# Performance work log

Measured on AMD Instinct MI355X. Metric: run time of the kernel, lower is better.

The kernel has to match this reference:

```python
import jax, jax.numpy as jnp
import numpy as np

B, T, C = 2, 2048, 2048
NH = 16            # query heads
NKV = NH // 2      # kv heads (GQA)
HD = C // NH       # head dim = 128
N_REP = NH // NKV  # 2


def setup_inputs() -> dict:
    key = jax.random.key(0)
    k1, k2, k3 = jax.random.split(key, 3)
    x = jax.random.normal(k1, (B, T, C), jnp.float32)
    w_attn = jax.random.normal(k2, (C, (NH + 2 * NKV) * HD), jnp.float32) * 0.02
    w_proj = jax.random.normal(k3, (C, C), jnp.float32) * 0.02
    t = jnp.arange(T, dtype=jnp.float32)
    inv_freq = 1.0 / (10000.0 ** (jnp.arange(0, HD, 2, dtype=jnp.float32) / HD))
    freqs = t[:, None] * inv_freq[None, :]  # [T, HD//2]
    return {"x": x, "w_attn": w_attn, "w_proj": w_proj,
            "freqs_cos": jnp.cos(freqs), "freqs_sin": jnp.sin(freqs)}


def _rope(v, cos, sin):
    # v: [B, T, H, HD]; complex multiply on (even, odd) pairs
    vr = v.reshape(*v.shape[:-1], HD // 2, 2)
    x0, x1 = vr[..., 0], vr[..., 1]
    c = cos[None, :, None, :]
    s = sin[None, :, None, :]
    o0 = x0 * c - x1 * s
    o1 = x0 * s + x1 * c
    return jnp.stack([o0, o1], axis=-1).reshape(v.shape)


def reference(x, w_attn, w_proj, freqs_cos, freqs_sin):
    qkv = x @ w_attn  # [B, T, (NH+2*NKV)*HD]
    q, k, v = jnp.split(qkv, [NH * HD, (NH + NKV) * HD], axis=-1)
    q = q.reshape(B, T, NH, HD)
    k = k.reshape(B, T, NKV, HD)
    v = v.reshape(B, T, NKV, HD)
    q = _rope(q, freqs_cos, freqs_sin)
    k = _rope(k, freqs_cos, freqs_sin)
    # GQA: group query heads over kv heads instead of repeating k/v
    q = q.transpose(0, 2, 1, 3).reshape(B, NKV, N_REP, T, HD)  # [B, G, R, T, HD]
    k = k.transpose(0, 2, 1, 3)  # [B, G, T, HD]
    v = v.transpose(0, 2, 1, 3)  # [B, G, T, HD]
    scale = jnp.float32(1.0 / np.sqrt(HD))
    scores = jnp.einsum('bgrqd,bgkd->bgrqk', q, k) * scale
    causal = jnp.tril(jnp.ones((T, T), dtype=bool))
    scores = jnp.where(causal, scores, jnp.float32(-1e30))
    p = jax.nn.softmax(scores, axis=-1)
    y = jnp.einsum('bgrqk,bgkd->bgrqd', p, v)  # [B, G, R, T, HD]
    y = y.reshape(B, NH, T, HD).transpose(0, 2, 1, 3).reshape(B, T, C)
    return y @ w_proj
```

## Files before the change

### kernel.cpp

```cpp
#include <hip/hip_runtime.h>
#include <hip/hip_bf16.h>
#include <stdint.h>
#include <stddef.h>

typedef unsigned short u16;
using bf16x8 = __attribute__((ext_vector_type(8))) short;
using f32x4  = __attribute__((ext_vector_type(4))) float;

#define DEVFN static __device__ __forceinline__

DEVFN u16 f2b(float f){ __hip_bfloat16 h = __float2bfloat16(f); return *reinterpret_cast<u16*>(&h); }
DEVFN float b2f(u16 u){ __hip_bfloat16 h; *reinterpret_cast<u16*>(&h) = u; return __bfloat162float(h); }

DEVFN void gload_lds16(const void* g, void* l){
  __builtin_amdgcn_global_load_lds(
      (const __attribute__((address_space(1))) void*)g,
      (__attribute__((address_space(3))) void*)l, 16, 0, 0);
}

__global__ void detect_k(const uint32_t* __restrict__ fc_raw, uint32_t* __restrict__ flag){
  if (threadIdx.x == 0 && blockIdx.x == 0)
    flag[0] = (fc_raw[0] == 0x3F800000u) ? 1u : 0u;
}

__global__ __launch_bounds__(256) void cvtf_k(const void* __restrict__ in, float* __restrict__ out,
                                              int n, const uint32_t* __restrict__ flag){
  const int i = blockIdx.x*256 + threadIdx.x;
  if (i >= n) return;
  if (flag[0]) out[i] = ((const float*)in)[i];
  else         out[i] = b2f(((const u16*)in)[i]);
}

__global__ __launch_bounds__(256) void cvtx_k(const void* __restrict__ in, u16* __restrict__ out,
                                              int n8, const uint32_t* __restrict__ flag){
  const int i = blockIdx.x*256 + threadIdx.x;
  if (i >= n8) return;
  __align__(16) u16 e[8];
  if (flag[0]){
    const float* f = (const float*)in + (size_t)i*8;
    float4 a = *(const float4*)f, b = *(const float4*)(f+4);
    e[0]=f2b(a.x); e[1]=f2b(a.y); e[2]=f2b(a.z); e[3]=f2b(a.w);
    e[4]=f2b(b.x); e[5]=f2b(b.y); e[6]=f2b(b.z); e[7]=f2b(b.w);
  } else {
    *(uint4*)e = *((const uint4*)in + i);
  }
  *(uint4*)(out + (size_t)i*8) = *(const uint4*)e;
}

__global__ __launch_bounds__(512) void wtrans_k(const void* __restrict__ in, u16* __restrict__ out,
                                                int C, int R, const uint32_t* __restrict__ flag){
  __shared__ __align__(16) u16 tile[64][72];
  const int r0 = blockIdx.y*64, c0 = blockIdx.x*64;
  const int t = threadIdx.x, r = t>>3, cs = (t&7)*8;
  __align__(16) u16 e[8];
  if (flag[0]){
    const float* f = (const float*)in + (size_t)(r0+r)*C + c0 + cs;
    float4 a = *(const float4*)f, b = *(const float4*)(f+4);
    e[0]=f2b(a.x); e[1]=f2b(a.y); e[2]=f2b(a.z); e[3]=f2b(a.w);
    e[4]=f2b(b.x); e[5]=f2b(b.y); e[6]=f2b(b.z); e[7]=f2b(b.w);
  } else {
    *(uint4*)e = *(const uint4*)((const u16*)in + (size_t)(r0+r)*C + c0 + cs);
  }
#pragma unroll
  for (int j=0;j<8;j++) tile[cs+j][r] = e[j];
  __syncthreads();
  uint4 o = *(const uint4*)&tile[r][cs];
  *(uint4*)(out + (size_t)(c0+r)*R + r0 + cs) = o;
}

__global__ __launch_bounds__(512) void vtrans_k(const u16* __restrict__ qkv, u16* __restrict__ vT){
  __shared__ __align__(16) u16 tile[64][72];
  const int z = blockIdx.z, b = z>>3, g = z&7;
  const u16* in = qkv + (size_t)(b*2048)*4096 + 3072 + g*128;
  u16* out = vT + (size_t)z*128*2048;
  const int r0 = blockIdx.y*64, c0 = blockIdx.x*64;
  const int t = threadIdx.x, r = t>>3, cs = (t&7)*8;
  uint4 v = *(const uint4*)(in + (size_t)(r0+r)*4096 + c0 + cs);
  const u16* e = (const u16*)&v;
#pragma unroll
  for (int j=0;j<8;j++) tile[cs+j][r] = e[j];
  __syncthreads();
  uint4 o = *(const uint4*)&tile[r][cs];
  *(uint4*)(out + (size_t)(c0+r)*2048 + r0 + cs) = o;
}

__global__ __launch_bounds__(256) void rope_k(u16* qkv, const float* __restrict__ fc,
                                              const float* __restrict__ fs){
  const int idx = blockIdx.x*256 + threadIdx.x;
  const int row = idx / 1536;
  const int p   = idx % 1536;
  const int col0 = p*2;
  const int t = row & 2047;
  const int i = p & 63;
  uint32_t* ptr = (uint32_t*)(qkv + (size_t)row*4096 + col0);
  uint32_t u = *ptr;
  float x0 = b2f((u16)(u & 0xffff));
  float x1 = b2f((u16)(u >> 16));
  float c = fc[t*64+i], s = fs[t*64+i];
  float o0 = x0*c - x1*s;
  float o1 = x0*s + x1*c;
  *ptr = (uint32_t)f2b(o0) | ((uint32_t)f2b(o1) << 16);
}

__global__ __launch_bounds__(256) void gemm_bt(const u16* __restrict__ A, const u16* __restrict__ Bt,
                                               void* __restrict__ Cv, int M, int N, int K,
                                               const uint32_t* __restrict__ flag, int fin){
  __shared__ __align__(16) u16 Al[2][128*32];
  __shared__ __align__(16) u16 Bl[2][128*32];
  const int nwg_x = N>>7;
  int wg = blockIdx.x;
  {
    const int nwg = gridDim.x;
    const int cpx = nwg >> 3;
    wg = (wg & 7)*cpx + (wg >> 3);
  }
  const int tm = (wg / nwg_x)*128, tn = (wg % nwg_x)*128;
  const int tid = threadIdx.x, w = tid>>6, l = tid&63, lr = l&15, lg = l>>4;
  const int wr = w>>1, wc = w&1;

  f32x4 acc[4][4] = {};

  auto stage = [&](int buf, int kk){
#pragma unroll
    for (int issue=0; issue<2; ++issue){
      const int c = issue*256 + w*64 + l;
      const int r = c>>2, sl = c&3;
      const int gch = sl ^ (r&3);
      gload_lds16(A  + (size_t)(tm + r)*K + kk + gch*8, &Al[buf][(issue*256 + w*64)*8]);
      gload_lds16(Bt + (size_t)(tn + r)*K + kk + gch*8, &Bl[buf][(issue*256 + w*64)*8]);
    }
  };

  stage(0, 0);
  __syncthreads();
  const int nk = K>>5;
  for (int kt=0; kt<nk; ++kt){
    if (kt+1 < nk) stage((kt+1)&1, (kt+1)*32);
    const u16* Ab = Al[kt&1];
    const u16* Bb = Bl[kt&1];
    bf16x8 a[4], b[4];
#pragma unroll
    for (int mi=0;mi<4;mi++){
      const int rr = wr*64 + mi*16 + lr;
      a[mi] = *(const bf16x8*)&Ab[rr*32 + ((lg ^ (rr&3))*8)];
    }
#pragma unroll
    for (int ni=0;ni<4;ni++){
      const int rr = wc*64 + ni*16 + lr;
      b[ni] = *(const bf16x8*)&Bb[rr*32 + ((lg ^ (rr&3))*8)];
    }
#pragma unroll
    for (int mi=0;mi<4;mi++)
#pragma unroll
      for (int ni=0;ni<4;ni++)
        acc[mi][ni] = __builtin_amdgcn_mfma_f32_16x16x32_bf16(a[mi], b[ni], acc[mi][ni], 0,0,0);
    __syncthreads();
  }
  const bool of32 = fin && (flag[0] != 0);
#pragma unroll
  for (int mi=0;mi<4;mi++)
#pragma unroll
    for (int ni=0;ni<4;ni++)
#pragma unroll
      for (int reg=0;reg<4;reg++){
        const int row = tm + wr*64 + mi*16 + lg*4 + reg;
        const int col = tn + wc*64 + ni*16 + lr;
        const size_t idx = (size_t)row*N + col;
        const float v = acc[mi][ni][reg];
        if (of32) ((float*)Cv)[idx] = v;
        else      ((u16*)Cv)[idx]   = f2b(v);
      }
}

__global__ __launch_bounds__(512) void attn_k(const u16* __restrict__ qkv, const u16* __restrict__ vT,
                                              u16* __restrict__ y){
  __shared__ __align__(16) u16 Kl[128*128];
  __shared__ __align__(16) u16 Vl[128*128];
  __shared__ __align__(16) u16 Pl[8][16][132];
  const int i0 = blockIdx.x;
  const int g  = i0 & 7;
  const int s  = i0 >> 3;
  const int b  = s >> 4;
  const int h  = g*2 + (s & 1);
  const int vq = (s >> 1) & 7;
  const int tid = threadIdx.x, w = tid>>6, l = tid&63, lr = l&15, lg = l>>4;
  const float scale = 0.08838834764831845f;

  const u16* kg = qkv + (size_t)(b*2048)*4096 + 2048 + g*128;
  const u16* vg = vT  + (size_t)(b*8+g)*128*2048;

  const int rk = tid >> 2;
  const int cb = tid & 3;
  u16* klp[4]; u16* vlp[4];
#pragma unroll
  for (int j=0;j<4;j++){
    const int ch = cb + j*4;
    klp[j] = &Kl[rk*128 + ((ch ^ (rk&15))*8)];
    vlp[j] = &Vl[rk*128 + ((ch ^ (rk&15))*8)];
  }
  uint4 kpre[4], vpre[4];

  const int nA = vq + 1;
  auto loadt = [&](int it){
    const int kb = ((it < nA) ? it : it - nA) * 128;
#pragma unroll
    for (int j=0;j<4;j++){
      kpre[j] = *(const uint4*)(kg + (size_t)(kb + rk)*4096 + (cb + j*4)*8);
      vpre[j] = *(const uint4*)(vg + (size_t)rk*2048 + kb + (cb + j*4)*8);
    }
  };
  auto writet = [&](){
#pragma unroll
    for (int j=0;j<4;j++){ *(uint4*)klp[j] = kpre[j]; *(uint4*)vlp[j] = vpre[j]; }
  };

  loadt(0); writet(); __syncthreads();

  bf16x8 aq[4];
  f32x4 yacc[8];
  float mrow[4], lsum[4];
  int qt = vq;
  auto loadQ = [&](){
    const size_t qrow = (size_t)(b*2048 + qt*128 + w*16 + lr);
#pragma unroll
    for (int c=0;c<4;c++)
      aq[c] = *(const bf16x8*)(qkv + qrow*4096 + h*128 + c*32 + lg*8);
  };
  auto resetAcc = [&](){
#pragma unroll
    for (int n=0;n<8;n++) yacc[n] = f32x4{0.f,0.f,0.f,0.f};
#pragma unroll
    for (int r=0;r<4;r++){ mrow[r] = -1e30f; lsum[r] = 0.f; }
  };
  auto writeOut = [&](){
    float inv[4];
#pragma unroll
    for (int r=0;r<4;r++) inv[r] = 1.f/lsum[r];
    const int qbase = b*2048 + qt*128 + w*16;
#pragma unroll
    for (int n=0;n<8;n++)
#pragma unroll
      for (int r=0;r<4;r++)
        y[(size_t)(qbase + lg*4 + r)*2048 + h*128 + n*16 + lr] = f2b(yacc[n][r]*inv[r]);
  };
  loadQ(); resetAcc();

  for (int it=0; it<17; ++it){
    const int kt = (it < nA) ? it : it - nA;
    const int kb = kt*128;
    const bool diag = (kt == qt);
    if (it+1 < 17) loadt(it+1);

    f32x4 sc[8];
#pragma unroll
    for (int n=0;n<8;n++) sc[n] = f32x4{0.f,0.f,0.f,0.f};
    __builtin_amdgcn_s_setprio(1);
#pragma unroll
    for (int c=0;c<4;c++)
#pragma unroll
      for (int ng=0; ng<8; ++ng){
        const int n = ng*16 + lr;
        bf16x8 bk = *(const bf16x8*)&Kl[n*128 + (((c*4+lg) ^ (n&15))*8)];
        sc[ng] = __builtin_amdgcn_mfma_f32_16x16x32_bf16(aq[c], bk, sc[ng], 0,0,0);
      }
    __builtin_amdgcn_s_setprio(0);

    float corr[4];
#pragma unroll
    for (int r=0;r<4;r++){
      const int qg = qt*128 + w*16 + lg*4 + r;
      float vmax = -1e30f;
#pragma unroll
      for (int ng=0; ng<8; ++ng){
        float v0 = sc[ng][r]*scale;
        if (diag && (kb + ng*16 + lr) > qg) v0 = -1e30f;
        sc[ng][r] = v0;
        vmax = fmaxf(vmax, v0);
      }
#pragma unroll
      for (int mm=1; mm<16; mm<<=1) vmax = fmaxf(vmax, __shfl_xor(vmax, mm));
      const float mnew = fmaxf(mrow[r], vmax);
      corr[r] = __expf(mrow[r] - mnew);
      mrow[r] = mnew;
      float sum = 0.f;
#pragma unroll
      for (int ng=0; ng<8; ++ng){
        const float p = __expf(sc[ng][r] - mnew);
        sc[ng][r] = p; sum += p;
      }
#pragma unroll
      for (int mm=1; mm<16; mm<<=1) sum += __shfl_xor(sum, mm);
      lsum[r] = lsum[r]*corr[r] + sum;
    }
#pragma unroll
    for (int n=0;n<8;n++)
#pragma unroll
      for (int r=0;r<4;r++) yacc[n][r] *= corr[r];

#pragma unroll
    for (int ng=0; ng<8; ++ng)
#pragma unroll
      for (int r=0;r<4;r++)
        Pl[w][lg*4+r][ng*16+lr] = f2b(sc[ng][r]);
    asm volatile("s_waitcnt lgkmcnt(0)" ::: "memory");
    __builtin_amdgcn_sched_barrier(0);
    bf16x8 ap[4];
#pragma unroll
    for (int kc=0;kc<4;kc++)
      ap[kc] = *(const bf16x8*)&Pl[w][lr][kc*32 + lg*8];

    __builtin_amdgcn_s_setprio(1);
#pragma unroll
    for (int n=0;n<8;n++)
#pragma unroll
      for (int kc=0;kc<4;kc++){
        const int d = n*16 + lr;
        bf16x8 bv = *(const bf16x8*)&Vl[d*128 + (((kc*4+lg) ^ (d&15))*8)];
        yacc[n] = __builtin_amdgcn_mfma_f32_16x16x32_bf16(ap[kc], bv, yacc[n], 0,0,0);
      }
    __builtin_amdgcn_s_setprio(0);

    if (it == nA-1){
      writeOut();
      qt = 15 - vq;
      loadQ(); resetAcc();
    }
    __syncthreads();
    if (it+1 < 17) writet();
    __syncthreads();
  }
  writeOut();
}

extern "C" void kernel_launch(void* const* d_in, const int* in_sizes, int n_in,
                              void* d_out, int out_size, void* d_ws, size_t ws_size,
                              hipStream_t stream){
  char* ws = (char*)d_ws;
  const size_t MB = 1048576;
  uint32_t* flag = (uint32_t*)(ws);
  float* fcF = (float*)(ws + 1*MB);
  float* fsF = (float*)(ws + 1*MB + 524288);
  u16* xb   = (u16*)(ws + 2*MB);
  u16* waT  = (u16*)(ws + 18*MB);
  u16* wpT  = (u16*)(ws + 34*MB);
  u16* qkvb = (u16*)(ws + 42*MB);
  u16* vTb  = (u16*)(ws + 74*MB);
  u16* yb   = xb;

  detect_k<<<1, 64, 0, stream>>>((const uint32_t*)d_in[3], flag);
  cvtf_k  <<<512, 256, 0, stream>>>(d_in[3], fcF, 131072, flag);
  cvtf_k  <<<512, 256, 0, stream>>>(d_in[4], fsF, 131072, flag);
  cvtx_k  <<<4096, 256, 0, stream>>>(d_in[0], xb, 1048576, flag);
  wtrans_k<<<dim3(64,32,1), 512, 0, stream>>>(d_in[1], waT, 4096, 2048, flag);
  wtrans_k<<<dim3(32,32,1), 512, 0, stream>>>(d_in[2], wpT, 2048, 2048, flag);
  gemm_bt <<<dim3(1024,1,1), 256, 0, stream>>>(xb, waT, qkvb, 4096, 4096, 2048, flag, 0);
  rope_k  <<<dim3(24576,1,1), 256, 0, stream>>>(qkvb, fcF, fsF);
  vtrans_k<<<dim3(2,32,16), 512, 0, stream>>>(qkvb, vTb);
  attn_k  <<<dim3(256,1,1), 512, 0, stream>>>(qkvb, vTb, yb);
  gemm_bt <<<dim3(512,1,1), 256, 0, stream>>>(yb, wpT, d_out, 4096, 2048, 2048, flag, 1);
}
```

Before: 319.0 us.

## Restructure attention kernel with 32x32 MFMA, KV-split warp groups and register-resident P

Rewrites the flash-attention kernel so each 128-key tile is split between two warp groups of 64 keys each, using 32x32x16 MFMAs with transposed (S^T) scores. The P matrix now stays in registers through cross-lane shuffles instead of round-tripping through LDS, and double-buffered K/V LDS tiles remove one barrier per iteration. A lazy rescale skips the accumulator correction when the row max grows by at most 8. Fully masked tiles are skipped. The two groups' partial outputs are merged through LDS at the end, which adds bf16 rounding of the partials and extra synchronisation.

After: 303.8 us. 1.05x faster.

```diff
diff --git a/kernel.cpp b/kernel.cpp
--- a/kernel.cpp
+++ b/kernel.cpp
@@ -6,6 +6,7 @@
 typedef unsigned short u16;
 using bf16x8 = __attribute__((ext_vector_type(8))) short;
 using f32x4  = __attribute__((ext_vector_type(4))) float;
+using f32x16 = __attribute__((ext_vector_type(16))) float;
 
 #define DEVFN static __device__ __forceinline__
 
@@ -172,164 +173,247 @@
       }
 }
 
-__global__ __launch_bounds__(512) void attn_k(const u16* __restrict__ qkv, const u16* __restrict__ vT,
-                                              u16* __restrict__ y){
-  __shared__ __align__(16) u16 Kl[128*128];
-  __shared__ __align__(16) u16 Vl[128*128];
-  __shared__ __align__(16) u16 Pl[8][16][132];
+__global__ __launch_bounds__(512, 2) void attn_k(const u16* __restrict__ qkv,
+                                                 const u16* __restrict__ vT,
+                                                 u16* __restrict__ y){
+  __shared__ __align__(16) u16 KV[2][2][16384];
   const int i0 = blockIdx.x;
   const int g  = i0 & 7;
-  const int s  = i0 >> 3;
-  const int b  = s >> 4;
-  const int h  = g*2 + (s & 1);
-  const int vq = (s >> 1) & 7;
-  const int tid = threadIdx.x, w = tid>>6, l = tid&63, lr = l&15, lg = l>>4;
+  const int r1 = i0 >> 3;
+  const int hl = r1 & 1;
+  const int vq = (r1 >> 1) & 7;
+  const int b  = r1 >> 4;
+  const int h  = g*2 + hl;
+
+  const int tid = threadIdx.x;
+  const int w = tid >> 6, l = tid & 63;
+  const int grp = w >> 2, wq = w & 3;
+  const int lq = l & 31;
+  const int hi = l >> 5;
   const float scale = 0.08838834764831845f;
 
   const u16* kg = qkv + (size_t)(b*2048)*4096 + 2048 + g*128;
   const u16* vg = vT  + (size_t)(b*8+g)*128*2048;
 
-  const int rk = tid >> 2;
-  const int cb = tid & 3;
-  u16* klp[4]; u16* vlp[4];
-#pragma unroll
-  for (int j=0;j<4;j++){
-    const int ch = cb + j*4;
-    klp[j] = &Kl[rk*128 + ((ch ^ (rk&15))*8)];
-    vlp[j] = &Vl[rk*128 + ((ch ^ (rk&15))*8)];
-  }
+  const int rk = tid >> 2, cb = tid & 3;
   uint4 kpre[4], vpre[4];
-
+  auto loadT = [&](int kvbase){
+#pragma unroll
+    for (int j=0;j<4;j++){
+      const int ch = cb + j*4;
+      kpre[j] = *(const uint4*)(kg + (size_t)(kvbase + rk)*4096 + ch*8);
+      vpre[j] = *(const uint4*)(vg + (size_t)rk*2048 + kvbase + ch*8);
+    }
+  };
+  auto writeT = [&](int buf){
+    u16* Kd = &KV[buf][rk>>6][0];
+    const int rl = rk & 63;
+#pragma unroll
+    for (int j=0;j<4;j++){
+      const int ch = cb + j*4;
+      *(uint4*)&Kd[rl*128 + ((ch ^ (rl&15))*8)] = kpre[j];
+    }
+#pragma unroll
+    for (int j=0;j<4;j++){
+      const int ch = cb + j*4;
+      u16* Vd = &KV[buf][ch>>3][8192];
+      *(uint4*)&Vd[rk*64 + (((ch&7) ^ (rk&7))*8)] = vpre[j];
+    }
+  };
+
+  int qt = vq;
   const int nA = vq + 1;
-  auto loadt = [&](int it){
-    const int kb = ((it < nA) ? it : it - nA) * 128;
-#pragma unroll
-    for (int j=0;j<4;j++){
-      kpre[j] = *(const uint4*)(kg + (size_t)(kb + rk)*4096 + (cb + j*4)*8);
-      vpre[j] = *(const uint4*)(vg + (size_t)rk*2048 + kb + (cb + j*4)*8);
-    }
-  };
-  auto writet = [&](){
-#pragma unroll
-    for (int j=0;j<4;j++){ *(uint4*)klp[j] = kpre[j]; *(uint4*)vlp[j] = vpre[j]; }
-  };
-
-  loadt(0); writet(); __syncthreads();
-
-  bf16x8 aq[4];
-  f32x4 yacc[8];
-  float mrow[4], lsum[4];
-  int qt = vq;
-  auto loadQ = [&](){
-    const size_t qrow = (size_t)(b*2048 + qt*128 + w*16 + lr);
-#pragma unroll
-    for (int c=0;c<4;c++)
-      aq[c] = *(const bf16x8*)(qkv + qrow*4096 + h*128 + c*32 + lg*8);
-  };
-  auto resetAcc = [&](){
-#pragma unroll
-    for (int n=0;n<8;n++) yacc[n] = f32x4{0.f,0.f,0.f,0.f};
-#pragma unroll
-    for (int r=0;r<4;r++){ mrow[r] = -1e30f; lsum[r] = 0.f; }
-  };
-  auto writeOut = [&](){
-    float inv[4];
-#pragma unroll
-    for (int r=0;r<4;r++) inv[r] = 1.f/lsum[r];
-    const int qbase = b*2048 + qt*128 + w*16;
-#pragma unroll
-    for (int n=0;n<8;n++)
-#pragma unroll
-      for (int r=0;r<4;r++)
-        y[(size_t)(qbase + lg*4 + r)*2048 + h*128 + n*16 + lr] = f2b(yacc[n][r]*inv[r]);
-  };
+  bf16x8 qf[8];
+  f32x16 yacc[4];
+  float mrow, lsum;
+
+  auto loadQ = [&]{
+    const size_t qrow = (size_t)(b*2048 + qt*128 + wq*32 + lq);
+    const u16* qp = qkv + qrow*4096 + h*128 + hi*8;
+#pragma unroll
+    for (int ds=0; ds<8; ++ds) qf[ds] = *(const bf16x8*)(qp + ds*16);
+  };
+  auto resetAcc = [&]{
+#pragma unroll
+    for (int dt=0; dt<4; ++dt)
+#pragma unroll
+      for (int r=0; r<16; ++r) yacc[dt][r] = 0.f;
+    mrow = -1e30f; lsum = 0.f;
+  };
+
+  auto mergePhase = [&](u16* Mb){
+    float* Mm = (float*)Mb; float* Ml = Mm + 128;
+    u16* MOs = Mb + 512 + wq*4096;
+    __syncthreads();
+    if (grp == 1){
+      if (l < 32){ Mm[wq*32 + l] = mrow; Ml[wq*32 + l] = lsum; }
+#pragma unroll
+      for (int dt=0; dt<4; ++dt)
+#pragma unroll
+        for (int rq=0; rq<4; ++rq){
+          const int d0 = dt*32 + rq*8 + hi*4;
+          uint32_t lo = (uint32_t)f2b(yacc[dt][rq*4+0]) | ((uint32_t)f2b(yacc[dt][rq*4+1])<<16);
+          uint32_t hi2= (uint32_t)f2b(yacc[dt][rq*4+2]) | ((uint32_t)f2b(yacc[dt][rq*4+3])<<16);
+          const int idx = (lq*128 + d0) ^ ((lq&7)<<3);
+          *(uint2*)&MOs[idx] = make_uint2(lo, hi2);
+        }
+    }
+    __syncthreads();
+    if (grp == 0){
+      const float mo = Mm[wq*32 + lq], lo_ = Ml[wq*32 + lq];
+      const float ms = fmaxf(mrow, mo);
+      const float ce = __expf(mrow - ms), co = __expf(mo - ms);
+      const float inv = 1.f / (lsum*ce + lo_*co);
+#pragma unroll
+      for (int dt=0; dt<4; ++dt)
+#pragma unroll
+        for (int rq=0; rq<4; ++rq){
+          const int d0 = dt*32 + rq*8 + hi*4;
+          const int idx = (lq*128 + d0) ^ ((lq&7)<<3);
+          uint2 pr = *(const uint2*)&MOs[idx];
+          const float yo0 = b2f((u16)(pr.x & 0xffff)), yo1 = b2f((u16)(pr.x >> 16));
+          const float yo2 = b2f((u16)(pr.y & 0xffff)), yo3 = b2f((u16)(pr.y >> 16));
+          const float f0 = (yacc[dt][rq*4+0]*ce + yo0*co)*inv;
+          const float f1 = (yacc[dt][rq*4+1]*ce + yo1*co)*inv;
+          const float f2v= (yacc[dt][rq*4+2]*ce + yo2*co)*inv;
+          const float f3 = (yacc[dt][rq*4+3]*ce + yo3*co)*inv;
+          uint32_t lo = (uint32_t)f2b(f0) | ((uint32_t)f2b(f1)<<16);
+          uint32_t hi2= (uint32_t)f2b(f2v)| ((uint32_t)f2b(f3)<<16);
+          *(uint2*)&MOs[idx] = make_uint2(lo, hi2);
+        }
+    }
+    __syncthreads();
+    const int qb2 = b*2048 + qt*128 + wq*32;
+#pragma unroll
+    for (int p=0; p<2; ++p){
+      const int row = grp*16 + p*8 + (l>>3);
+      const int gc = l & 7;
+      const int idx0 = (row*128 + gc*16) ^ ((row&7)<<3);
+      const int idx1 = (row*128 + gc*16 + 8) ^ ((row&7)<<3);
+      uint4 v0 = *(const uint4*)&MOs[idx0];
+      uint4 v1 = *(const uint4*)&MOs[idx1];
+      u16* yp = y + (size_t)(qb2 + row)*2048 + h*128 + gc*16;
+      *(uint4*)yp = v0;
+      *(uint4*)(yp + 8) = v1;
+    }
+    __syncthreads();
+  };
+
+  loadT(0); writeT(0); __syncthreads();
   loadQ(); resetAcc();
 
-  for (int it=0; it<17; ++it){
-    const int kt = (it < nA) ? it : it - nA;
-    const int kb = kt*128;
-    const bool diag = (kt == qt);
-    if (it+1 < 17) loadt(it+1);
-
-    f32x4 sc[8];
-#pragma unroll
-    for (int n=0;n<8;n++) sc[n] = f32x4{0.f,0.f,0.f,0.f};
-    __builtin_amdgcn_s_setprio(1);
-#pragma unroll
-    for (int c=0;c<4;c++)
-#pragma unroll
-      for (int ng=0; ng<8; ++ng){
-        const int n = ng*16 + lr;
-        bf16x8 bk = *(const bf16x8*)&Kl[n*128 + (((c*4+lg) ^ (n&15))*8)];
-        sc[ng] = __builtin_amdgcn_mfma_f32_16x16x32_bf16(aq[c], bk, sc[ng], 0,0,0);
-      }
-    __builtin_amdgcn_s_setprio(0);
-
-    float corr[4];
-#pragma unroll
-    for (int r=0;r<4;r++){
-      const int qg = qt*128 + w*16 + lg*4 + r;
-      float vmax = -1e30f;
-#pragma unroll
-      for (int ng=0; ng<8; ++ng){
-        float v0 = sc[ng][r]*scale;
-        if (diag && (kb + ng*16 + lr) > qg) v0 = -1e30f;
-        sc[ng][r] = v0;
-        vmax = fmaxf(vmax, v0);
-      }
-#pragma unroll
-      for (int mm=1; mm<16; mm<<=1) vmax = fmaxf(vmax, __shfl_xor(vmax, mm));
-      const float mnew = fmaxf(mrow[r], vmax);
-      corr[r] = __expf(mrow[r] - mnew);
-      mrow[r] = mnew;
-      float sum = 0.f;
-#pragma unroll
-      for (int ng=0; ng<8; ++ng){
-        const float p = __expf(sc[ng][r] - mnew);
-        sc[ng][r] = p; sum += p;
-      }
-#pragma unroll
-      for (int mm=1; mm<16; mm<<=1) sum += __shfl_xor(sum, mm);
-      lsum[r] = lsum[r]*corr[r] + sum;
-    }
-#pragma unroll
-    for (int n=0;n<8;n++)
-#pragma unroll
-      for (int r=0;r<4;r++) yacc[n][r] *= corr[r];
-
-#pragma unroll
-    for (int ng=0; ng<8; ++ng)
-#pragma unroll
-      for (int r=0;r<4;r++)
-        Pl[w][lg*4+r][ng*16+lr] = f2b(sc[ng][r]);
-    asm volatile("s_waitcnt lgkmcnt(0)" ::: "memory");
-    __builtin_amdgcn_sched_barrier(0);
-    bf16x8 ap[4];
-#pragma unroll
-    for (int kc=0;kc<4;kc++)
-      ap[kc] = *(const bf16x8*)&Pl[w][lr][kc*32 + lg*8];
-
-    __builtin_amdgcn_s_setprio(1);
-#pragma unroll
-    for (int n=0;n<8;n++)
-#pragma unroll
-      for (int kc=0;kc<4;kc++){
-        const int d = n*16 + lr;
-        bf16x8 bv = *(const bf16x8*)&Vl[d*128 + (((kc*4+lg) ^ (d&15))*8)];
-        yacc[n] = __builtin_amdgcn_mfma_f32_16x16x32_bf16(ap[kc], bv, yacc[n], 0,0,0);
-      }
-    __builtin_amdgcn_s_setprio(0);
-
-    if (it == nA-1){
-      writeOut();
+  for (int s=0; s<17; ++s){
+    if (s == nA){
+      mergePhase(&KV[(nA&1)^1][0][0]);
       qt = 15 - vq;
       loadQ(); resetAcc();
     }
-    __syncthreads();
-    if (it+1 < 17) writet();
+    const int sj = (s < nA) ? s : s - nA;
+    const int kvbase = sj*128;
+    if (s+1 < 17){
+      const int s2 = s+1;
+      const int sj2 = (s2 < nA) ? s2 : s2 - nA;
+      loadT(sj2*128);
+    }
+    const u16* Kb = &KV[s&1][grp][0];
+    const u16* Vb = Kb + 8192;
+    const int tilebase = kvbase + grp*64;
+    const int qmin = qt*128 + wq*32;
+    const int qrow = qmin + lq;
+
+    if (tilebase <= qmin + 31){
+      f32x16 sc[2];
+#pragma unroll
+      for (int t=0;t<2;t++)
+#pragma unroll
+        for (int r=0;r<16;r++) sc[t][r] = 0.f;
+      __builtin_amdgcn_s_setprio(1);
+#pragma unroll
+      for (int t=0; t<2; ++t){
+        const int r = t*32 + lq;
+        const int rsw = r & 15;
+#pragma unroll
+        for (int ds=0; ds<8; ++ds){
+          const bf16x8 kf = *(const bf16x8*)&Kb[r*128 + (((2*ds+hi) ^ rsw)*8)];
+          sc[t] = __builtin_amdgcn_mfma_f32_32x32x16_bf16(kf, qf[ds], sc[t], 0,0,0);
+        }
+      }
+      __builtin_amdgcn_s_setprio(0);
+
+      const bool needmask = (tilebase + 63) > qmin;
+      float pmax = -1e30f;
+#pragma unroll
+      for (int t=0;t<2;t++)
+#pragma unroll
+        for (int r=0;r<16;r++){
+          float v = sc[t][r]*scale;
+          if (needmask){
+            const int kp = tilebase + t*32 + (r&3) + 8*(r>>2) + 4*hi;
+            if (kp > qrow) v = -1e30f;
+          }
+          sc[t][r] = v;
+          pmax = fmaxf(pmax, v);
+        }
+      pmax = fmaxf(pmax, __shfl_xor(pmax, 32));
+      if (!__all(pmax <= mrow + 8.f)){
+        const float mnew = fmaxf(mrow, pmax);
+        const float corr = __expf(mrow - mnew);
+        mrow = mnew; lsum *= corr;
+#pragma unroll
+        for (int dt=0;dt<4;dt++)
+#pragma unroll
+          for (int r=0;r<16;r++) yacc[dt][r] *= corr;
+      }
+      float lsub = 0.f;
+#pragma unroll
+      for (int t=0;t<2;t++)
+#pragma unroll
+        for (int r=0;r<16;r++){
+          const float p = __expf(sc[t][r] - mrow);
+          sc[t][r] = p; lsub += p;
+        }
+      lsub += __shfl_xor(lsub, 32);
+      lsum += lsub;
+
+      __align__(16) uint32_t pw[4][4];
+#pragma unroll
+      for (int t=0;t<2;t++)
+#pragma unroll
+        for (int half=0; half<2; ++half){
+          const int q8 = half*8;
+          uint32_t X0 = (uint32_t)f2b(sc[t][q8+0]) | ((uint32_t)f2b(sc[t][q8+1])<<16);
+          uint32_t X1 = (uint32_t)f2b(sc[t][q8+2]) | ((uint32_t)f2b(sc[t][q8+3])<<16);
+          uint32_t X2 = (uint32_t)f2b(sc[t][q8+4]) | ((uint32_t)f2b(sc[t][q8+5])<<16);
+          uint32_t X3 = (uint32_t)f2b(sc[t][q8+6]) | ((uint32_t)f2b(sc[t][q8+7])<<16);
+          const uint32_t pX0 = (uint32_t)__shfl_xor((int)X0, 32);
+          const uint32_t pX1 = (uint32_t)__shfl_xor((int)X1, 32);
+          const uint32_t pX2 = (uint32_t)__shfl_xor((int)X2, 32);
+          const uint32_t pX3 = (uint32_t)__shfl_xor((int)X3, 32);
+          const int ks = t*2 + half;
+          pw[ks][0] = hi ? pX2 : X0;
+          pw[ks][1] = hi ? pX3 : X1;
+          pw[ks][2] = hi ? X2 : pX0;
+          pw[ks][3] = hi ? X3 : pX1;
+        }
+
+      __builtin_amdgcn_s_setprio(1);
+#pragma unroll
+      for (int dt=0; dt<4; ++dt){
+        const int d = dt*32 + lq;
+        const int dsw = d & 7;
+#pragma unroll
+        for (int ks=0; ks<4; ++ks){
+          const bf16x8 vf = *(const bf16x8*)&Vb[8192 - 8192 + d*64 + (((2*ks+hi) ^ dsw)*8)];
+          yacc[dt] = __builtin_amdgcn_mfma_f32_32x32x16_bf16(vf, *(const bf16x8*)&pw[ks][0], yacc[dt], 0,0,0);
+        }
+      }
+      __builtin_amdgcn_s_setprio(0);
+    }
+
+    if (s+1 < 17) writeT((s&1)^1);
     __syncthreads();
   }
-  writeOut();
+  mergePhase(&KV[0][0][0]);
 }
 
 extern "C" void kernel_launch(void* const* d_in, const int* in_sizes, int n_in,
```
